# Optimization experiments

Measured on AMD Instinct MI355X. Metric: run time of the kernel, lower is better.

## Reference

```python
import jax, jax.numpy as jnp
import numpy as np

N_HEADS = 16
N_KV_HEADS = 4
HEAD_DIM = 128


def _rope(x, cos, sin):
    # x: [b, s, h, d]; cos/sin: [s, d//2]; interleaved pair rotation
    b, s, h, d = x.shape
    xp = x.reshape(b, s, h, d // 2, 2)
    x_r, x_i = xp[..., 0], xp[..., 1]
    c = cos[None, :, None, :]
    sn = sin[None, :, None, :]
    o_r = x_r * c - x_i * sn
    o_i = x_r * sn + x_i * c
    return jnp.stack([o_r, o_i], axis=-1).reshape(b, s, h, d)


def setup_inputs() -> dict:
    key = jax.random.key(0)
    ks = jax.random.split(key, 7)
    B, S, D = 2, 2048, 2048
    KV = N_KV_HEADS * HEAD_DIM
    x = jax.random.normal(ks[0], (B, S, D), dtype=jnp.float32)
    freqs_cos = jax.random.uniform(ks[1], (S, HEAD_DIM // 2), dtype=jnp.float32)
    freqs_sin = jax.random.uniform(ks[2], (S, HEAD_DIM // 2), dtype=jnp.float32)
    scale = 0.02
    wq = jax.random.normal(ks[3], (D, D), dtype=jnp.float32) * scale
    wk = jax.random.normal(ks[4], (KV, D), dtype=jnp.float32) * scale
    wv = jax.random.normal(ks[5], (KV, D), dtype=jnp.float32) * scale
    wo = jax.random.normal(ks[6], (D, D), dtype=jnp.float32) * scale
    return {"x": x, "freqs_cos": freqs_cos, "freqs_sin": freqs_sin,
            "wq": wq, "wk": wk, "wv": wv, "wo": wo}


def reference(x, freqs_cos, freqs_sin, wq, wk, wv, wo):
    B, S, D = x.shape
    n_rep = N_HEADS // N_KV_HEADS
    q = (x @ wq.T).reshape(B, S, N_HEADS, HEAD_DIM)
    k = (x @ wk.T).reshape(B, S, N_KV_HEADS, HEAD_DIM)
    v = (x @ wv.T).reshape(B, S, N_KV_HEADS, HEAD_DIM)
    q = _rope(q, freqs_cos, freqs_sin)
    k = _rope(k, freqs_cos, freqs_sin)
    # repeat_kv == torch.repeat_interleave along head dim
    k = jnp.repeat(k, n_rep, axis=2)
    v = jnp.repeat(v, n_rep, axis=2)
    q = q.transpose(0, 2, 1, 3)  # [B, H, S, d]
    k = k.transpose(0, 2, 1, 3)
    v = v.transpose(0, 2, 1, 3)
    scale = 1.0 / np.sqrt(HEAD_DIM).astype(np.float32)
    scores = jnp.einsum('bhqd,bhkd->bhqk', q, k) * scale
    causal = jnp.tril(jnp.ones((S, S), dtype=bool))
    scores = jnp.where(causal[None, None], scores, jnp.finfo(jnp.float32).min)
    probs = jax.nn.softmax(scores.astype(jnp.float32), axis=-1).astype(q.dtype)
    out = jnp.einsum('bhqk,bhkd->bhqd', probs, v)
    out = out.transpose(0, 2, 1, 3).reshape(B, S, N_HEADS * HEAD_DIM)
    return out @ wo.T
```

## Files before the change

kernel.cpp:

```cpp
#include <hip/hip_runtime.h>
#include <hip/hip_bf16.h>
#include <type_traits>

using bf16x8 = __attribute__((ext_vector_type(8))) short;
using f32x4  = __attribute__((ext_vector_type(4))) float;
using u16x8  = __attribute__((ext_vector_type(8))) unsigned short;
using u16x4  = __attribute__((ext_vector_type(4))) unsigned short;
using u32x4  = __attribute__((ext_vector_type(4))) unsigned int;

__device__ __forceinline__ float b2f(unsigned short u) {
    unsigned int x = ((unsigned int)u) << 16;
    return __builtin_bit_cast(float, x);
}
__device__ __forceinline__ unsigned short f2b(float f) {
    __hip_bfloat16 h = __float2bfloat16(f);
    return __builtin_bit_cast(unsigned short, h);
}

__device__ __forceinline__ void async_copy16(const void* g, void* l) {
    __builtin_amdgcn_global_load_lds(
        (const __attribute__((address_space(1))) unsigned int*)g,
        (__attribute__((address_space(3))) unsigned int*)l, 16, 0, 0);
}

#define MFMA16(a, b, c) __builtin_amdgcn_mfma_f32_16x16x32_bf16(a, b, c, 0, 0, 0)

__global__ __launch_bounds__(256) void cvt_f32_to_bf16(
    const float* __restrict__ s, unsigned short* __restrict__ d, int n4)
{
    int i = blockIdx.x * blockDim.x + threadIdx.x;
    if (i >= n4) return;
    float4 v = ((const float4*)s)[i];
    ushort4 o;
    o.x = f2b(v.x); o.y = f2b(v.y); o.z = f2b(v.z); o.w = f2b(v.w);
    ((ushort4*)d)[i] = o;
}

__global__ __launch_bounds__(256) void qkv_gemm(
    const unsigned short* __restrict__ A,
    const unsigned short* __restrict__ Wq,
    const unsigned short* __restrict__ Wk,
    const unsigned short* __restrict__ Wv,
    unsigned short* __restrict__ Q,
    unsigned short* __restrict__ Kk,
    unsigned short* __restrict__ V)
{
    const int K = 2048;
    constexpr int BK = 64;
    __shared__ unsigned short As[128 * BK];
    __shared__ unsigned short Bs[128 * BK];

    int tid  = threadIdx.x;
    int w    = tid >> 6;
    int lane = tid & 63;
    int idx  = lane & 15;
    int quad = lane >> 4;
    int wm   = (w >> 1) * 64;
    int wn   = (w & 1) * 64;

    int bm = blockIdx.x / 24;
    int bn = blockIdx.x - bm * 24;
    int m0 = bm * 128;

    const unsigned short* Bt;
    unsigned short* C;
    int Nc, n0;
    if (bn < 16)      { Bt = Wq + (size_t)bn * 128 * K;        C = Q;  Nc = 2048; n0 = bn * 128; }
    else if (bn < 20) { Bt = Wk + (size_t)(bn - 16) * 128 * K; C = Kk; Nc = 512;  n0 = (bn - 16) * 128; }
    else              { Bt = Wv + (size_t)(bn - 20) * 128 * K; C = V;  Nc = 512;  n0 = (bn - 20) * 128; }

    int srow   = lane >> 3;
    int schunk = (lane & 7) ^ srow;

    f32x4 acc[4][4];
    #pragma unroll
    for (int mi = 0; mi < 4; ++mi)
        #pragma unroll
        for (int ni = 0; ni < 4; ++ni) acc[mi][ni] = (f32x4){0.f, 0.f, 0.f, 0.f};

    for (int k0 = 0; k0 < K; k0 += BK) {
        #pragma unroll
        for (int i = 0; i < 4; ++i) {
            int cb = w * 4 + i;
            size_t goff = (size_t)(cb * 8 + srow) * K + k0 + schunk * 8;
            async_copy16(A + (size_t)m0 * K + goff, &As[cb * 512]);
            async_copy16(Bt + goff, &Bs[cb * 512]);
        }
        __syncthreads();

        #pragma unroll
        for (int ks = 0; ks < 2; ++ks) {
            bf16x8 af[4], bfr[4];
            #pragma unroll
            for (int mi = 0; mi < 4; ++mi) {
                int row = wm + mi * 16 + idx;
                af[mi] = *(const bf16x8*)&As[row * BK + (((ks * 4 + quad) ^ (row & 7)) * 8)];
            }
            #pragma unroll
            for (int ni = 0; ni < 4; ++ni) {
                int row = wn + ni * 16 + idx;
                bfr[ni] = *(const bf16x8*)&Bs[row * BK + (((ks * 4 + quad) ^ (row & 7)) * 8)];
            }
            #pragma unroll
            for (int mi = 0; mi < 4; ++mi)
                #pragma unroll
                for (int ni = 0; ni < 4; ++ni)
                    acc[mi][ni] = MFMA16(af[mi], bfr[ni], acc[mi][ni]);
        }
        __syncthreads();
    }

    #pragma unroll
    for (int mi = 0; mi < 4; ++mi) {
        #pragma unroll
        for (int r = 0; r < 4; ++r) {
            size_t row = (size_t)(m0 + wm + mi * 16 + quad * 4 + r);
            #pragma unroll
            for (int ni = 0; ni < 4; ++ni) {
                int col = n0 + wn + ni * 16 + idx;
                C[row * Nc + col] = f2b(acc[mi][ni][r]);
            }
        }
    }
}

template <typename OutT>
__global__ __launch_bounds__(256) void gemm_tile(
    const unsigned short* __restrict__ A,
    const unsigned short* __restrict__ Bt,
    OutT* __restrict__ C,
    int M, int N, int K)
{
    constexpr int BK = 64;
    __shared__ unsigned short As[128 * BK];
    __shared__ unsigned short Bs[128 * BK];

    int tid  = threadIdx.x;
    int w    = tid >> 6;
    int lane = tid & 63;
    int idx  = lane & 15;
    int quad = lane >> 4;
    int wm   = (w >> 1) * 64;
    int wn   = (w & 1) * 64;

    int tilesN = N / 128;
    int bm = blockIdx.x / tilesN;
    int bn = blockIdx.x - bm * tilesN;
    int m0 = bm * 128, n0 = bn * 128;

    int srow   = lane >> 3;
    int schunk = (lane & 7) ^ srow;

    f32x4 acc[4][4];
    #pragma unroll
    for (int mi = 0; mi < 4; ++mi)
        #pragma unroll
        for (int ni = 0; ni < 4; ++ni) acc[mi][ni] = (f32x4){0.f, 0.f, 0.f, 0.f};

    for (int k0 = 0; k0 < K; k0 += BK) {
        #pragma unroll
        for (int i = 0; i < 4; ++i) {
            int cb = w * 4 + i;
            size_t goff = (size_t)(cb * 8 + srow) * K + k0 + schunk * 8;
            async_copy16(A  + (size_t)m0 * K + goff, &As[cb * 512]);
            async_copy16(Bt + (size_t)n0 * K + goff, &Bs[cb * 512]);
        }
        __syncthreads();

        #pragma unroll
        for (int ks = 0; ks < 2; ++ks) {
            bf16x8 af[4], bfr[4];
            #pragma unroll
            for (int mi = 0; mi < 4; ++mi) {
                int row = wm + mi * 16 + idx;
                af[mi] = *(const bf16x8*)&As[row * BK + (((ks * 4 + quad) ^ (row & 7)) * 8)];
            }
            #pragma unroll
            for (int ni = 0; ni < 4; ++ni) {
                int row = wn + ni * 16 + idx;
                bfr[ni] = *(const bf16x8*)&Bs[row * BK + (((ks * 4 + quad) ^ (row & 7)) * 8)];
            }
            #pragma unroll
            for (int mi = 0; mi < 4; ++mi)
                #pragma unroll
                for (int ni = 0; ni < 4; ++ni)
                    acc[mi][ni] = MFMA16(af[mi], bfr[ni], acc[mi][ni]);
        }
        __syncthreads();
    }

    #pragma unroll
    for (int mi = 0; mi < 4; ++mi) {
        #pragma unroll
        for (int r = 0; r < 4; ++r) {
            size_t row = (size_t)(m0 + wm + mi * 16 + quad * 4 + r);
            #pragma unroll
            for (int ni = 0; ni < 4; ++ni) {
                int col = n0 + wn + ni * 16 + idx;
                if constexpr (std::is_same_v<OutT, float>) {
                    C[row * N + col] = acc[mi][ni][r];
                } else {
                    C[row * N + col] = f2b(acc[mi][ni][r]);
                }
            }
        }
    }
}

__global__ __launch_bounds__(256) void rope_kernel(
    unsigned short* __restrict__ x,
    const float* __restrict__ cs,
    const float* __restrict__ sn,
    int H, int total, float oscale)
{
    int e = blockIdx.x * blockDim.x + threadIdx.x;
    if (e >= total) return;
    int i = e & 63;
    int s = (e / (64 * H)) & 2047;
    float xr = b2f(x[2 * e]);
    float xi = b2f(x[2 * e + 1]);
    float c  = cs[s * 64 + i];
    float sv = sn[s * 64 + i];
    x[2 * e]     = f2b((xr * c - xi * sv) * oscale);
    x[2 * e + 1] = f2b((xr * sv + xi * c) * oscale);
}

__global__ __launch_bounds__(512, 4) void flash_attn(
    const unsigned short* __restrict__ qg,
    const unsigned short* __restrict__ kk,
    const unsigned short* __restrict__ vv,
    unsigned short* __restrict__ out)
{
    const int S = 2048;
    int bid = blockIdx.x;
    int qp  = bid & 15;
    int bh  = bid >> 4;
    int h   = bh & 15;
    int b   = bh >> 4;
    int kvh = h >> 2;

    int tid  = threadIdx.x;
    int w    = tid >> 6;
    int lane = tid & 63;
    int idx  = lane & 15;
    int quad = lane >> 4;

    int qt  = (w >> 2) ? (31 - qp) : qp;
    int q0  = qt * 64;
    int wq0 = q0 + (w & 3) * 16;
    int qr  = wq0 + idx;

    __shared__ unsigned short Ks[32 * 128];
    __shared__ unsigned short Vt[128 * 40];

    const unsigned short* kbase = kk + ((size_t)b * S * 4 + kvh) * 128;
    const unsigned short* vbase = vv + ((size_t)b * S * 4 + kvh) * 128;

    bf16x8 qf[4];
    {
        const unsigned short* qpp =
            qg + ((size_t)((b * S + wq0 + idx) * 16 + h)) * 128 + quad * 8;
        #pragma unroll
        for (int ko = 0; ko < 4; ++ko)
            qf[ko] = *(const bf16x8*)(qpp + ko * 32);
    }

    f32x4 acc[8];
    #pragma unroll
    for (int n = 0; n < 8; ++n) acc[n] = (f32x4){0.f, 0.f, 0.f, 0.f};
    float lsum = 0.f;

    int dp = (tid & 63) * 2;
    int jb = (tid >> 6) & 3;
    int ih = (tid >> 8) * 4;

    int ntA = 2 * qp + 2, ntB = 64 - 2 * qp;
    int nt  = ntA > ntB ? ntA : ntB;

    for (int t = 0; t < nt; ++t) {
        {
            int key = w * 4 + (lane >> 4);
            int sc  = (lane & 15) ^ (key & 7);
            async_copy16(kbase + ((size_t)(t * 32 + key)) * 512 + sc * 8,
                         &Ks[w * 512]);
        }
        {
            const unsigned short* vc = vbase + ((size_t)(t * 32 + jb * 4)) * 512 + dp;
            unsigned int ld[4];
            #pragma unroll
            for (int i = 0; i < 4; ++i) {
                int ii  = ih + i;
                int key = (ii >> 1) + 16 * (ii & 1);
                ld[i] = *(const unsigned int*)(vc + key * 512);
            }
            u16x4 lo, hi;
            #pragma unroll
            for (int i = 0; i < 4; ++i) {
                lo[i] = (unsigned short)ld[i];
                hi[i] = (unsigned short)(ld[i] >> 16);
            }
            *(u16x4*)&Vt[dp * 40 + jb * 8 + ih]       = lo;
            *(u16x4*)&Vt[(dp + 1) * 40 + jb * 8 + ih] = hi;
        }
        __syncthreads();

        if (t * 32 <= wq0 + 15) {
            f32x4 s0 = {0.f,0.f,0.f,0.f}, s1 = {0.f,0.f,0.f,0.f};
            #pragma unroll
            for (int ko = 0; ko < 4; ++ko) {
                int kc = ko * 4 + quad;
                bf16x8 kf0 = *(const bf16x8*)&Ks[idx * 128 + ((kc ^ (idx & 7)) * 8)];
                bf16x8 kf1 = *(const bf16x8*)&Ks[(16 + idx) * 128 + ((kc ^ (idx & 7)) * 8)];
                s0 = MFMA16(kf0, qf[ko], s0);
                s1 = MFMA16(kf1, qf[ko], s1);
            }
            unsigned int pk[4];
            if (t * 32 + 31 <= wq0) {
                #pragma unroll
                for (int r = 0; r < 4; ++r) {
                    float p0 = exp2f(s0[r]);
                    float p1 = exp2f(s1[r]);
                    lsum += p0 + p1;
                    pk[r] = (unsigned int)f2b(p0) | ((unsigned int)f2b(p1) << 16);
                }
            } else {
                int L = qr - t * 32;
                #pragma unroll
                for (int r = 0; r < 4; ++r) {
                    int kl = quad * 4 + r;
                    float p0 = (kl      <= L) ? exp2f(s0[r]) : 0.f;
                    float p1 = (kl + 16 <= L) ? exp2f(s1[r]) : 0.f;
                    lsum += p0 + p1;
                    pk[r] = (unsigned int)f2b(p0) | ((unsigned int)f2b(p1) << 16);
                }
            }
            u32x4 pku = {pk[0], pk[1], pk[2], pk[3]};
            bf16x8 pf = __builtin_bit_cast(bf16x8, pku);
            #pragma unroll
            for (int n = 0; n < 8; ++n) {
                bf16x8 vf = *(const bf16x8*)&Vt[(n * 16 + idx) * 40 + quad * 8];
                acc[n] = MFMA16(vf, pf, acc[n]);
            }
        }
        __syncthreads();
    }

    lsum += __shfl_xor(lsum, 16);
    lsum += __shfl_xor(lsum, 32);
    float inv = 1.f / lsum;
    size_t rowb = (size_t)(b * S + wq0 + idx) * 2048 + h * 128;
    #pragma unroll
    for (int n = 0; n < 8; ++n) {
        ushort4 o;
        o.x = f2b(acc[n][0] * inv);
        o.y = f2b(acc[n][1] * inv);
        o.z = f2b(acc[n][2] * inv);
        o.w = f2b(acc[n][3] * inv);
        *(ushort4*)&out[rowb + n * 16 + quad * 4] = o;
    }
}

extern "C" void kernel_launch(void* const* d_in, const int* in_sizes, int n_in,
                              void* d_out, int out_size, void* d_ws, size_t ws_size,
                              hipStream_t stream)
{
    const float* x  = (const float*)d_in[0];
    const float* fc = (const float*)d_in[1];
    const float* fs = (const float*)d_in[2];
    const float* wq = (const float*)d_in[3];
    const float* wk = (const float*)d_in[4];
    const float* wv = (const float*)d_in[5];
    const float* wo = (const float*)d_in[6];
    float* out = (float*)d_out;

    const int B = 2, S = 2048, D = 2048, KV = 512;
    const int M = B * S;

    unsigned short* ws  = (unsigned short*)d_ws;
    unsigned short* xb  = ws;
    unsigned short* wqb = xb  + (size_t)M * D;
    unsigned short* wkb = wqb + (size_t)D * D;
    unsigned short* wvb = wkb + (size_t)KV * D;
    unsigned short* wob = wvb + (size_t)KV * D;
    unsigned short* qb  = wob + (size_t)D * D;
    unsigned short* kb  = qb  + (size_t)M * D;
    unsigned short* vb  = kb  + (size_t)M * KV;
    unsigned short* ao  = vb  + (size_t)M * KV;

    cvt_f32_to_bf16<<<dim3((M * D / 4) / 256), dim3(256), 0, stream>>>(x,  xb,  M * D / 4);
    cvt_f32_to_bf16<<<dim3((D * D / 4) / 256), dim3(256), 0, stream>>>(wq, wqb, D * D / 4);
    cvt_f32_to_bf16<<<dim3((KV * D / 4) / 256), dim3(256), 0, stream>>>(wk, wkb, KV * D / 4);
    cvt_f32_to_bf16<<<dim3((KV * D / 4) / 256), dim3(256), 0, stream>>>(wv, wvb, KV * D / 4);
    cvt_f32_to_bf16<<<dim3((D * D / 4) / 256), dim3(256), 0, stream>>>(wo, wob, D * D / 4);

    qkv_gemm<<<dim3(768), dim3(256), 0, stream>>>(xb, wqb, wkb, wvb, qb, kb, vb);

    int qpairs = B * S * 16 * 64;
    int kpairs = B * S * 4 * 64;
    const float c2 = 0.12752584f;
    rope_kernel<<<dim3(qpairs / 256), dim3(256), 0, stream>>>(qb, fc, fs, 16, qpairs, c2);
    rope_kernel<<<dim3(kpairs / 256), dim3(256), 0, stream>>>(kb, fc, fs, 4, kpairs, 1.0f);

    flash_attn<<<dim3(512), dim3(512), 0, stream>>>(qb, kb, vb, ao);

    gemm_tile<float><<<dim3((M / 128) * (D / 128)), dim3(256), 0, stream>>>(ao, wob, out, M, D, D);
}
```

Measured before the change: 337.6 us.

## Rebalance causal attention work across batches, swizzle V tile, use raw exp2

```diff
diff --git a/kernel.cpp b/kernel.cpp
--- a/kernel.cpp
+++ b/kernel.cpp
@@ -16,6 +16,16 @@
     __hip_bfloat16 h = __float2bfloat16(f);
     return __builtin_bit_cast(unsigned short, h);
 }
+
+#if defined(__has_builtin)
+#if __has_builtin(__builtin_amdgcn_exp2f)
+#define EXP2F(x) __builtin_amdgcn_exp2f(x)
+#else
+#define EXP2F(x) exp2f(x)
+#endif
+#else
+#define EXP2F(x) exp2f(x)
+#endif
 
 __device__ __forceinline__ void async_copy16(const void* g, void* l) {
     __builtin_amdgcn_global_load_lds(
@@ -239,13 +249,15 @@
     int b   = bh >> 4;
     int kvh = h >> 2;
 
+    int p   = b ? (15 - qp) : qp;
+
     int tid  = threadIdx.x;
     int w    = tid >> 6;
     int lane = tid & 63;
     int idx  = lane & 15;
     int quad = lane >> 4;
 
-    int qt  = (w >> 2) ? (31 - qp) : qp;
+    int qt  = 2 * p + (w >> 2);
     int q0  = qt * 64;
     int wq0 = q0 + (w & 3) * 16;
     int qr  = wq0 + idx;
@@ -274,8 +286,9 @@
     int jb = (tid >> 6) & 3;
     int ih = (tid >> 8) * 4;
 
-    int ntA = 2 * qp + 2, ntB = 64 - 2 * qp;
-    int nt  = ntA > ntB ? ntA : ntB;
+    int vcol = (((jb ^ ((dp >> 3) & 3)) << 3) + ih);
+
+    int nt = 4 * p + 4;
 
     for (int t = 0; t < nt; ++t) {
         {
@@ -299,8 +312,8 @@
                 lo[i] = (unsigned short)ld[i];
                 hi[i] = (unsigned short)(ld[i] >> 16);
             }
-            *(u16x4*)&Vt[dp * 40 + jb * 8 + ih]       = lo;
-            *(u16x4*)&Vt[(dp + 1) * 40 + jb * 8 + ih] = hi;
+            *(u16x4*)&Vt[dp * 40 + vcol]       = lo;
+            *(u16x4*)&Vt[(dp + 1) * 40 + vcol] = hi;
         }
         __syncthreads();
 
@@ -318,8 +331,8 @@
             if (t * 32 + 31 <= wq0) {
                 #pragma unroll
                 for (int r = 0; r < 4; ++r) {
-                    float p0 = exp2f(s0[r]);
-                    float p1 = exp2f(s1[r]);
+                    float p0 = EXP2F(s0[r]);
+                    float p1 = EXP2F(s1[r]);
                     lsum += p0 + p1;
                     pk[r] = (unsigned int)f2b(p0) | ((unsigned int)f2b(p1) << 16);
                 }
@@ -328,8 +341,8 @@
                 #pragma unroll
                 for (int r = 0; r < 4; ++r) {
                     int kl = quad * 4 + r;
-                    float p0 = (kl      <= L) ? exp2f(s0[r]) : 0.f;
-                    float p1 = (kl + 16 <= L) ? exp2f(s1[r]) : 0.f;
+                    float p0 = (kl      <= L) ? EXP2F(s0[r]) : 0.f;
+                    float p1 = (kl + 16 <= L) ? EXP2F(s1[r]) : 0.f;
                     lsum += p0 + p1;
                     pk[r] = (unsigned int)f2b(p0) | ((unsigned int)f2b(p1) << 16);
                 }
@@ -338,7 +351,8 @@
             bf16x8 pf = __builtin_bit_cast(bf16x8, pku);
             #pragma unroll
             for (int n = 0; n < 8; ++n) {
-                bf16x8 vf = *(const bf16x8*)&Vt[(n * 16 + idx) * 40 + quad * 8];
+                int rr = n * 16 + idx;
+                bf16x8 vf = *(const bf16x8*)&Vt[rr * 40 + ((quad ^ ((rr >> 3) & 3)) << 3)];
                 acc[n] = MFMA16(vf, pf, acc[n]);
             }
         }
```

New measurement: 332.5 us. Within noise of the previous version (-1.5%).
